# Optimization experiments

Measured on AMD Instinct MI355X. Metric: run time of the kernel, lower is better.

## Reference

```python
import jax, jax.numpy as jnp
import numpy as np

HEADS = 4
DIM_HEAD = 64
SCALE = 8.0
EPS = 1e-5  # fp32 branch of the original LayerNorm


def setup_inputs() -> dict:
    key = jax.random.key(0)
    k1, k2, k3 = jax.random.split(key, 3)
    B, C, F, H, W = 2, 256, 4, 32, 32
    inner = HEADS * DIM_HEAD  # 256
    x = jax.random.normal(k1, (B, C, F, H, W), dtype=jnp.float32)
    gamma = jnp.ones((1, C, 1, 1, 1), dtype=jnp.float32)
    w_qkv = jax.random.normal(k2, (3 * inner, C), dtype=jnp.float32) * 0.05
    w_out = jax.random.normal(k3, (C, inner), dtype=jnp.float32) * 0.05
    return {"x": x, "gamma": gamma, "w_qkv": w_qkv, "w_out": w_out}


def _l2norm(t):
    return t / jnp.sqrt(jnp.sum(t * t, axis=-1, keepdims=True) + 1e-12)


def reference(x, gamma, w_qkv, w_out):
    B, C, F, H, W = x.shape
    N = F * H * W
    inner = HEADS * DIM_HEAD
    residual = x

    # channel LayerNorm (biased variance over dim=1)
    mean = jnp.mean(x, axis=1, keepdims=True)
    var = jnp.mean((x - mean) ** 2, axis=1, keepdims=True)
    xn = (x - mean) / jnp.sqrt(var + EPS) * gamma

    # 1x1x1 conv == channel matmul; flatten spatial dims to sequence
    xn_flat = xn.reshape(B, C, N)                      # [B, C, N]
    qkv = jnp.einsum('oc,bcn->bon', w_qkv, xn_flat)    # [B, 3*inner, N]
    qkv = qkv.reshape(B, 3, HEADS, DIM_HEAD, N)        # chunk then split heads
    qkv = jnp.transpose(qkv, (1, 0, 2, 4, 3))          # [3, B, h, N, d]
    q, k, v = qkv[0], qkv[1], qkv[2]

    q = _l2norm(q)
    k = _l2norm(k)

    sim = jnp.einsum('bhid,bhjd->bhij', q, k) * SCALE  # [B, h, N, N]
    attn = jax.nn.softmax(sim, axis=-1)
    out = jnp.einsum('bhij,bhjd->bhid', attn, v)       # [B, h, N, d]

    # 'b h n d -> b (h d) n' then 1x1x1 out conv
    out = jnp.transpose(out, (0, 1, 3, 2)).reshape(B, inner, N)
    out = jnp.einsum('oi,bin->bon', w_out, out).reshape(B, C, F, H, W)
    return out + residual
```

## Files before the change

### kernel.cpp

```cpp
#include <hip/hip_runtime.h>

#define BATCH 2
#define CCH   256
#define NSEQ  4096
#define NH    4
#define DH    64
#define INNER 256

typedef __attribute__((ext_vector_type(8))) __bf16 bf16x8;
typedef __attribute__((ext_vector_type(4))) float f32x4;
typedef __attribute__((ext_vector_type(8))) unsigned short u16x8;
typedef __attribute__((ext_vector_type(4))) unsigned short u16x4;

#define GLD16(gsrc, ldst)                                                     \
  __builtin_amdgcn_global_load_lds(                                           \
      (const __attribute__((address_space(1))) unsigned int*)(const void*)(gsrc), \
      (__attribute__((address_space(3))) unsigned int*)(void*)(ldst), 16, 0, 0)

static __device__ __forceinline__ unsigned short f2bfr(float f) {
  union { float f; unsigned u; } v; v.f = f;
  return (unsigned short)((v.u + 0x8000u) >> 16);
}
static __device__ __forceinline__ unsigned pack2(float f0, float f1) {
  union { float f; unsigned u; } a, b; a.f = f0; b.f = f1;
  return __builtin_amdgcn_perm(b.u + 0x8000u, a.u + 0x8000u, 0x07060302u);
}
static __device__ __forceinline__ unsigned cvtpk(float lo, float hi) {
  unsigned r;
  asm("v_cvt_pk_bf16_f32 %0, %1, %2" : "=v"(r) : "v"(lo), "v"(hi));
  return r;
}
static __device__ __forceinline__ float bf2f(unsigned short u) {
  union { unsigned u; float f; } v; v.u = ((unsigned)u) << 16;
  return v.f;
}
static __device__ __forceinline__ bf16x8 ldb(const unsigned short* p) {
  return *(const bf16x8*)p;
}
static __device__ __forceinline__ f32x4 mm(bf16x8 a, bf16x8 b, f32x4 c) {
  return __builtin_amdgcn_mfma_f32_16x16x32_bf16(a, b, c, 0, 0, 0);
}
static __device__ __forceinline__ float ex2(float x) {
  return __builtin_amdgcn_exp2f(x);
}

__global__ __launch_bounds__(256) void k_lncvt(const float* __restrict__ x,
                                               const float* __restrict__ gamma,
                                               unsigned short* __restrict__ xn,
                                               const float* __restrict__ wq,
                                               const float* __restrict__ wo,
                                               unsigned short* __restrict__ wqb,
                                               unsigned short* __restrict__ wob) {
  int blk = blockIdx.x;
  if (blk >= 256) {
    int t = (blk - 256) * 256 + threadIdx.x;
    int e = t * 4;
    if (e < 768 * 256) {
      float4 v = *(const float4*)(wq + e);
      u16x4 pk = { f2bfr(v.x), f2bfr(v.y), f2bfr(v.z), f2bfr(v.w) };
      *(u16x4*)(wqb + e) = pk;
    } else {
      int e2 = e - 768 * 256;
      float4 v = *(const float4*)(wo + e2);
      u16x4 pk = { f2bfr(v.x), f2bfr(v.y), f2bfr(v.z), f2bfr(v.w) };
      *(u16x4*)(wob + e2) = pk;
    }
    return;
  }
  int b  = blk >> 7;
  int n0 = (blk & 127) * 32;
  int t  = threadIdx.x;
  int nl = t & 31;
  int cg = t >> 5;
  int n  = n0 + nl;
  const float* xp = x + ((size_t)(b * CCH + cg * 32)) * NSEQ + n;
  float vals[32];
  float s = 0.f, s2 = 0.f;
#pragma unroll
  for (int j = 0; j < 32; j++) {
    float v = xp[(size_t)j * NSEQ];
    vals[j] = v; s += v; s2 += v * v;
  }
  __shared__ float rs[8][32], rs2[8][32];
  rs[cg][nl] = s; rs2[cg][nl] = s2;
  __syncthreads();
  float S = 0.f, S2 = 0.f;
#pragma unroll
  for (int g = 0; g < 8; g++) { S += rs[g][nl]; S2 += rs2[g][nl]; }
  float mean = S * (1.f / 256.f);
  float var  = S2 * (1.f / 256.f) - mean * mean;
  float rstd = rsqrtf(var + 1e-5f);
  unsigned short* dst = xn + ((size_t)b * NSEQ + n) * CCH + cg * 32;
#pragma unroll
  for (int j0 = 0; j0 < 32; j0 += 8) {
    u16x8 pk;
#pragma unroll
    for (int j = 0; j < 8; j++)
      pk[j] = f2bfr((vals[j0 + j] - mean) * rstd * gamma[cg * 32 + j0 + j]);
    *(u16x8*)(dst + j0) = pk;
  }
}

__global__ __launch_bounds__(256) void k_qkv(const unsigned short* __restrict__ wqb,
                                             const unsigned short* __restrict__ xn,
                                             unsigned short* __restrict__ qkv,
                                             unsigned short* __restrict__ qt,
                                             unsigned short* __restrict__ ktb) {
  int n0 = blockIdx.x * 64;
  int oi = blockIdx.y;
  int o0 = oi * 64;
  int b  = blockIdx.z;
  __shared__ unsigned short Al[64 * 128];
  __shared__ unsigned short Bl[64 * 128];
  int t = threadIdx.x;
  int lane = t & 63, w = t >> 6;
  int c = lane & 15, quad = lane >> 4;
  int wm = w >> 1, wn = w & 1;
  f32x4 acc[2][2] = {};
  int lr = lane >> 4;
  int lchk = lane & 15;
  const unsigned short* apg = wqb + (size_t)o0 * CCH;
  const unsigned short* bpg = xn + ((size_t)b * NSEQ + n0) * CCH;
  for (int kt = 0; kt < 2; kt++) {
    if (kt) __syncthreads();
#pragma unroll
    for (int q = 0; q < 4; q++) {
      int r = w * 16 + q * 4 + lr;
      int srcoff = r * CCH + kt * 128 + ((lchk ^ (r & 7)) * 8);
      GLD16(apg + srcoff, Al + (size_t)(w * 16 + q * 4) * 128);
      GLD16(bpg + srcoff, Bl + (size_t)(w * 16 + q * 4) * 128);
    }
    __syncthreads();
#pragma unroll
    for (int ks = 0; ks < 4; ks++) {
      int ra0 = wm * 32 + c, ra1 = ra0 + 16;
      int rb0 = wn * 32 + c, rb1 = rb0 + 16;
      bf16x8 a0 = ldb(&Al[ra0 * 128 + (((ks * 4 + quad) ^ (ra0 & 7)) * 8)]);
      bf16x8 a1 = ldb(&Al[ra1 * 128 + (((ks * 4 + quad) ^ (ra1 & 7)) * 8)]);
      bf16x8 b0 = ldb(&Bl[rb0 * 128 + (((ks * 4 + quad) ^ (rb0 & 7)) * 8)]);
      bf16x8 b1 = ldb(&Bl[rb1 * 128 + (((ks * 4 + quad) ^ (rb1 & 7)) * 8)]);
      acc[0][0] = mm(a0, b0, acc[0][0]);
      acc[0][1] = mm(a0, b1, acc[0][1]);
      acc[1][0] = mm(a1, b0, acc[1][0]);
      acc[1][1] = mm(a1, b1, acc[1][1]);
    }
  }
  if (oi < 8) {
    float* sq = (float*)Al;
    float s0 = 0.f, s1 = 0.f;
#pragma unroll
    for (int i = 0; i < 2; i++)
#pragma unroll
      for (int rr = 0; rr < 4; rr++) {
        s0 += acc[i][0][rr] * acc[i][0][rr];
        s1 += acc[i][1][rr] * acc[i][1][rr];
      }
    s0 += __shfl_xor(s0, 16); s0 += __shfl_xor(s0, 32);
    s1 += __shfl_xor(s1, 16); s1 += __shfl_xor(s1, 32);
    __syncthreads();
    if (quad == 0) {
      sq[wm * 64 + wn * 32 + c]      = s0;
      sq[wm * 64 + wn * 32 + 16 + c] = s1;
    }
    __syncthreads();
    float r0 = rsqrtf(sq[wn * 32 + c]      + sq[64 + wn * 32 + c]      + 1e-12f);
    float r1 = rsqrtf(sq[wn * 32 + 16 + c] + sq[64 + wn * 32 + 16 + c] + 1e-12f);
    if (oi < 4) { r0 *= 11.541560327111707f; r1 *= 11.541560327111707f; }
    int h = oi & 3;
    unsigned short* base = (oi < 4 ? qt : ktb) + ((size_t)(b * NH + h) * NSEQ) * DH;
#pragma unroll
    for (int i = 0; i < 2; i++)
#pragma unroll
      for (int j = 0; j < 2; j++) {
        float rsc = j ? r1 : r0;
        int n = n0 + wn * 32 + j * 16 + c;
        int d = wm * 32 + i * 16 + quad * 4;
        uint2 pk = { pack2(acc[i][j][0] * rsc, acc[i][j][1] * rsc),
                     pack2(acc[i][j][2] * rsc, acc[i][j][3] * rsc) };
        *(uint2*)(base + (size_t)n * DH + d) = pk;
      }
  } else {
#pragma unroll
    for (int i = 0; i < 2; i++)
#pragma unroll
      for (int j = 0; j < 2; j++)
#pragma unroll
        for (int rr = 0; rr < 4; rr++) {
          int o = o0 + wm * 32 + i * 16 + quad * 4 + rr;
          int n = n0 + wn * 32 + j * 16 + c;
          qkv[((size_t)b * 768 + o) * NSEQ + n] = f2bfr(acc[i][j][rr]);
        }
  }
}

__global__ __launch_bounds__(256, 2) void k_attn(
    const unsigned short* __restrict__ qt,
    const unsigned short* __restrict__ ktb,
    const unsigned short* __restrict__ qkv,
    unsigned short* __restrict__ opart,
    float* __restrict__ lpart,
    int S, int kvlen) {
  int i0 = blockIdx.x * 256;
  int h  = blockIdx.y;
  int bz = blockIdx.z;
  int b  = bz / S, s = bz % S;
  __shared__ unsigned short Kl[2][64 * 64];
  __shared__ unsigned short Vl[2][64 * 64];
  int t = threadIdx.x;
  int lane = t & 63, w = t >> 6;
  int c = lane & 15, quad = lane >> 4;

  const unsigned short* qbase = qt  + ((size_t)(b * NH + h) * NSEQ) * DH;
  const unsigned short* kbase = ktb + ((size_t)(b * NH + h) * NSEQ) * DH;
  const unsigned short* vbase = qkv + ((size_t)b * 768 + 512 + h * 64) * NSEQ;

  bf16x8 qa[4], qb[4];
#pragma unroll
  for (int ss = 0; ss < 4; ss++) {
    const unsigned short* qp =
        qbase + (size_t)(i0 + w * 64 + ss * 16 + c) * DH + quad * 8;
    qa[ss] = ldb(qp); qb[ss] = ldb(qp + 32);
  }

  u16x8 onesu;
#pragma unroll
  for (int j = 0; j < 8; j++) onesu[j] = 0x3F80;
  bf16x8 ones = *(bf16x8*)&onesu;

  f32x4 acc[4][4] = {};
  f32x4 accl[4]  = {};

  int slr = lane >> 3, slc = lane & 7;
  int ssw_v  = (slc ^ slr) * 8;
  int ssw_k1 = (slc ^ (slr & 3)) * 8;
  int ssw_k2 = ssw_k1 ^ 32;
  const unsigned short* kp = kbase + (size_t)(s * kvlen + w * 16 + slr) * DH;
  const unsigned short* vp = vbase + (size_t)(w * 16 + slr) * NSEQ + s * kvlen + ssw_v;
  int sw0 = (quad ^ (c & 7)) * 8;
  int sw1 = sw0 ^ 32;
  int fK    = (c & 3) | (((c >> 2) & 1) << 2);
  int swk0  = (quad ^ fK) * 8;
  int swk1  = swk0 ^ 32;
  int krow0 = (c >> 2) * 8 + (c & 3);

  int nIt = kvlen / 64;
  GLD16(kp + ssw_k1,          &Kl[0][(w * 16)     * 64]);
  GLD16(kp + 8 * DH + ssw_k2, &Kl[0][(w * 16 + 8) * 64]);
  kp += 64 * DH;

  union U4 { unsigned u[4]; bf16x8 v; };
  U4 pA0[4], pA1[4], pB0[4], pB1[4];

#define QKSET(qA, qB, P0, P1)                                                 \
  {                                                                           \
    f32x4 z0 = {}, z1 = {}, z2 = {}, z3 = {};                                 \
    __builtin_amdgcn_s_setprio(1);                                            \
    z0 = mm(k00, qA, z0); z0 = mm(k01, qB, z0);                               \
    z1 = mm(k10, qA, z1); z1 = mm(k11, qB, z1);                               \
    z2 = mm(k20, qA, z2); z2 = mm(k21, qB, z2);                               \
    z3 = mm(k30, qA, z3); z3 = mm(k31, qB, z3);                               \
    __builtin_amdgcn_s_setprio(0);                                            \
    P0.u[0] = cvtpk(ex2(z0[0]), ex2(z0[1]));                                  \
    P0.u[1] = cvtpk(ex2(z0[2]), ex2(z0[3]));                                  \
    P0.u[2] = cvtpk(ex2(z1[0]), ex2(z1[1]));                                  \
    P0.u[3] = cvtpk(ex2(z1[2]), ex2(z1[3]));                                  \
    P1.u[0] = cvtpk(ex2(z2[0]), ex2(z2[1]));                                  \
    P1.u[1] = cvtpk(ex2(z2[2]), ex2(z2[3]));                                  \
    P1.u[2] = cvtpk(ex2(z3[0]), ex2(z3[1]));                                  \
    P1.u[3] = cvtpk(ex2(z3[2]), ex2(z3[3]));                                  \
  }

#define PVD(dt, Vb, PO0, PO1)                                                 \
  {                                                                           \
    bf16x8 v0 = ldb(&Vb[((dt) * 16 + c) * 64 + sw0]);                         \
    bf16x8 v1 = ldb(&Vb[((dt) * 16 + c) * 64 + sw1]);                         \
    __builtin_amdgcn_s_setprio(1);                                            \
    acc[0][dt] = mm(PO0[0].v, v0, acc[0][dt]);                                \
    acc[0][dt] = mm(PO1[0].v, v1, acc[0][dt]);                                \
    acc[1][dt] = mm(PO0[1].v, v0, acc[1][dt]);                                \
    acc[1][dt] = mm(PO1[1].v, v1, acc[1][dt]);                                \
    acc[2][dt] = mm(PO0[2].v, v0, acc[2][dt]);                                \
    acc[2][dt] = mm(PO1[2].v, v1, acc[2][dt]);                                \
    acc[3][dt] = mm(PO0[3].v, v0, acc[3][dt]);                                \
    acc[3][dt] = mm(PO1[3].v, v1, acc[3][dt]);                                \
    __builtin_amdgcn_s_setprio(0);                                            \
  }

#define ACCL(PO0, PO1)                                                        \
  __builtin_amdgcn_s_setprio(1);                                              \
  accl[0] = mm(PO0[0].v, ones, accl[0]); accl[0] = mm(PO1[0].v, ones, accl[0]); \
  accl[1] = mm(PO0[1].v, ones, accl[1]); accl[1] = mm(PO1[1].v, ones, accl[1]); \
  accl[2] = mm(PO0[2].v, ones, accl[2]); accl[2] = mm(PO1[2].v, ones, accl[2]); \
  accl[3] = mm(PO0[3].v, ones, accl[3]); accl[3] = mm(PO1[3].v, ones, accl[3]); \
  __builtin_amdgcn_s_setprio(0);

#define ITER(IT, PN0, PN1, PO0, PO1, DO_PV)                                   \
  {                                                                           \
    __syncthreads();    \
    if ((IT) + 1 < nIt) {                                                     \
      unsigned short* kd = &Kl[((IT) + 1) & 1][0];                            \
      GLD16(kp + ssw_k1,          kd + (w * 16) * 64);                        \
      GLD16(kp + 8 * DH + ssw_k2, kd + (w * 16 + 8) * 64);                    \
      kp += 64 * DH;                                                          \
    }                                                                         \
    {                                                                         \
      unsigned short* vd = &Vl[(IT) & 1][0];                                  \
      GLD16(vp,            vd + (w * 16) * 64);                               \
      GLD16(vp + 8 * NSEQ, vd + (w * 16 + 8) * 64);                           \
      vp += 64;                                                               \
    }                                                                         \
    const unsigned short* Kb = &Kl[(IT) & 1][0];                              \
    const unsigned short* Vb = &Vl[((IT) + 1) & 1][0];       \
    bf16x8 k00 = ldb(&Kb[(krow0)      * 64 + swk0]);                          \
    bf16x8 k01 = ldb(&Kb[(krow0)      * 64 + swk1]);                          \
    bf16x8 k10 = ldb(&Kb[(krow0 + 4)  * 64 + swk0]);                          \
    bf16x8 k11 = ldb(&Kb[(krow0 + 4)  * 64 + swk1]);                          \
    bf16x8 k20 = ldb(&Kb[(krow0 + 32) * 64 + swk0]);                          \
    bf16x8 k21 = ldb(&Kb[(krow0 + 32) * 64 + swk1]);                          \
    bf16x8 k30 = ldb(&Kb[(krow0 + 36) * 64 + swk0]);                          \
    bf16x8 k31 = ldb(&Kb[(krow0 + 36) * 64 + swk1]);                          \
    QKSET(qa[0], qb[0], PN0[0], PN1[0]);                                      \
    if (DO_PV) PVD(0, Vb, PO0, PO1);                                          \
    QKSET(qa[1], qb[1], PN0[1], PN1[1]);                                      \
    if (DO_PV) PVD(1, Vb, PO0, PO1);                                          \
    QKSET(qa[2], qb[2], PN0[2], PN1[2]);                                      \
    if (DO_PV) PVD(2, Vb, PO0, PO1);                                          \
    QKSET(qa[3], qb[3], PN0[3], PN1[3]);                                      \
    if (DO_PV) PVD(3, Vb, PO0, PO1);                                          \
    if (DO_PV) { ACCL(PO0, PO1); }                                            \
  }

  for (int itp = 0; itp < nIt / 2; ++itp) {
    int it0 = itp * 2;
    ITER(it0,     pA0, pA1, pB0, pB1, (itp > 0));
    ITER(it0 + 1, pB0, pB1, pA0, pA1, 1);
  }
  __syncthreads();
  {
    const unsigned short* Vb = &Vl[1][0];
    PVD(0, Vb, pB0, pB1);
    PVD(1, Vb, pB0, pB1);
    PVD(2, Vb, pB0, pB1);
    PVD(3, Vb, pB0, pB1);
    ACCL(pB0, pB1);
  }
#undef ITER
#undef ACCL
#undef PVD
#undef QKSET

  size_t rb = ((size_t)(b * NH + h) * S + s) * NSEQ + i0 + w * 64;
#pragma unroll
  for (int ss = 0; ss < 4; ss++) {
    size_t rbs = rb + ss * 16;
    if (c == 0) {
#pragma unroll
      for (int rr = 0; rr < 4; rr++)
        lpart[rbs + quad * 4 + rr] = accl[ss][rr];
    }
#pragma unroll
    for (int rr = 0; rr < 4; rr++)
#pragma unroll
      for (int dt = 0; dt < 4; dt++)
        opart[(rbs + quad * 4 + rr) * 64 + dt * 16 + c] = f2bfr(acc[ss][dt][rr]);
  }
}

__global__ __launch_bounds__(256) void k_out(const unsigned short* __restrict__ wob,
                                             const unsigned short* __restrict__ opart,
                                             const float* __restrict__ lpart,
                                             const float* __restrict__ x,
                                             float* __restrict__ out, int S) {
  int n0 = blockIdx.x * 64;
  int o0 = blockIdx.y * 64;
  int b  = blockIdx.z;
  __shared__ unsigned short Al[64 * 256];
  __shared__ unsigned short Bl[64 * 256];
  int t = threadIdx.x;
  int lane = t & 63, w = t >> 6;
  int c = lane & 15, quad = lane >> 4;
  int wm = w >> 1, wn = w & 1;
  int lr2 = lane >> 5, lch = lane & 31;
  const unsigned short* apg = wob + (size_t)o0 * INNER;
#pragma unroll
  for (int q = 0; q < 8; q++) {
    int r = w * 16 + q * 2 + lr2;
    int srcoff = r * INNER + ((lch ^ (r & 7)) * 8);
    GLD16(apg + srcoff, Al + (size_t)(w * 16 + q * 2) * 256);
  }
  int n_l = t >> 2;
  int seg = t & 3;
#pragma unroll
  for (int hh = 0; hh < 4; hh++) {
    float l = 0.f;
    float o[16];
#pragma unroll
    for (int j = 0; j < 16; j++) o[j] = 0.f;
    for (int s = 0; s < S; s++) {
      size_t rbm = ((size_t)(b * NH + hh) * S + s) * NSEQ + n0 + n_l;
      l += lpart[rbm];
      const unsigned short* p = opart + rbm * 64 + seg * 16;
      u16x8 v0 = *(const u16x8*)p;
      u16x8 v1 = *(const u16x8*)(p + 8);
#pragma unroll
      for (int j = 0; j < 8; j++) {
        o[j]     += bf2f(v0[j]);
        o[8 + j] += bf2f(v1[j]);
      }
    }
    float inv = 1.f / l;
    int cc = hh * 8 + seg * 2;
    uint4 pkA = { pack2(o[0] * inv,  o[1] * inv),  pack2(o[2] * inv,  o[3] * inv),
                  pack2(o[4] * inv,  o[5] * inv),  pack2(o[6] * inv,  o[7] * inv) };
    uint4 pkB = { pack2(o[8] * inv,  o[9] * inv),  pack2(o[10] * inv, o[11] * inv),
                  pack2(o[12] * inv, o[13] * inv), pack2(o[14] * inv, o[15] * inv) };
    *(uint4*)&Bl[n_l * 256 + (((cc)     ^ (n_l & 7)) * 8)] = pkA;
    *(uint4*)&Bl[n_l * 256 + (((cc + 1) ^ (n_l & 7)) * 8)] = pkB;
  }
  __syncthreads();
  f32x4 acc[2][2] = {};
#pragma unroll
  for (int ks = 0; ks < 8; ks++) {
    int ra0 = wm * 32 + c, ra1 = ra0 + 16;
    int rb0 = wn * 32 + c, rb1 = rb0 + 16;
    bf16x8 a0 = ldb(&Al[ra0 * 256 + (((ks * 4 + quad) ^ (ra0 & 7)) * 8)]);
    bf16x8 a1 = ldb(&Al[ra1 * 256 + (((ks * 4 + quad) ^ (ra1 & 7)) * 8)]);
    bf16x8 b0 = ldb(&Bl[rb0 * 256 + (((ks * 4 + quad) ^ (rb0 & 7)) * 8)]);
    bf16x8 b1 = ldb(&Bl[rb1 * 256 + (((ks * 4 + quad) ^ (rb1 & 7)) * 8)]);
    acc[0][0] = mm(a0, b0, acc[0][0]);
    acc[0][1] = mm(a0, b1, acc[0][1]);
    acc[1][0] = mm(a1, b0, acc[1][0]);
    acc[1][1] = mm(a1, b1, acc[1][1]);
  }
#pragma unroll
  for (int i = 0; i < 2; i++)
#pragma unroll
    for (int j = 0; j < 2; j++)
#pragma unroll
      for (int rr = 0; rr < 4; rr++) {
        int o = o0 + wm * 32 + i * 16 + quad * 4 + rr;
        int n = n0 + wn * 32 + j * 16 + c;
        size_t idx = ((size_t)b * CCH + o) * NSEQ + n;
        out[idx] = acc[i][j][rr] + x[idx];
      }
}

extern "C" void kernel_launch(void* const* d_in, const int* in_sizes, int n_in,
                              void* d_out, int out_size, void* d_ws, size_t ws_size,
                              hipStream_t stream) {
  const float* x     = (const float*)d_in[0];
  const float* gamma = (const float*)d_in[1];
  const float* wq    = (const float*)d_in[2];
  const float* wo    = (const float*)d_in[3];
  float* out = (float*)d_out;

  const size_t MB = 1u << 20;
  char* ws = (char*)d_ws;
  unsigned short* xn  = (unsigned short*)(ws + 4 * MB);
  unsigned short* qkv = (unsigned short*)(ws + 8 * MB);
  unsigned short* wqb = (unsigned short*)(ws + 20 * MB);
  unsigned short* wob = (unsigned short*)(ws + 20 * MB + 512 * 1024);
  unsigned short* qt  = (unsigned short*)(ws + 21 * MB);
  unsigned short* ktb = (unsigned short*)(ws + 25 * MB);
  unsigned short* opart = (unsigned short*)(ws + 29 * MB);
  int S;
  if (ws_size >= 48 * MB) S = 4;
  else if (ws_size >= 40 * MB) S = 2;
  else S = 1;
  size_t opart_bytes = (size_t)S * BATCH * NH * NSEQ * DH * 2;
  float* lpart = (float*)(ws + 29 * MB + opart_bytes);
  int kvlen = NSEQ / S;

  k_lncvt<<<dim3(512),          256, 0, stream>>>(x, gamma, xn, wq, wo, wqb, wob);
  k_qkv  <<<dim3(64, 12, 2),    256, 0, stream>>>(wqb, xn, qkv, qt, ktb);
  k_attn <<<dim3(16, 4, 2 * S), 256, 0, stream>>>(qt, ktb, qkv, opart,
                                                  lpart, S, kvlen);
  k_out  <<<dim3(64, 4, 2),     256, 0, stream>>>(wob, opart, lpart, x, out, S);
}
```

Measured before the change: 128.1 us.

## Split split-KV merge into separate kernel and drop setprio hints in attention

Moves the split-KV partial merge and normalization out of the output projection kernel into a new k_merge kernel. k_merge writes a bf16 [B, N, inner] attention output to workspace. Previously each of the 4 output-channel blocks redid the merge for its tile. k_out now streams both operands with global_load_lds in two K-chunks, using half the shared memory. The change also removes the s_setprio raise/lower around the MFMA groups in the attention kernel, and adds one launch plus an intermediate round trip through memory.

```diff
diff --git a/kernel.cpp b/kernel.cpp
--- a/kernel.cpp
+++ b/kernel.cpp
@@ -254,12 +254,10 @@
 #define QKSET(qA, qB, P0, P1)                                                 \
   {                                                                           \
     f32x4 z0 = {}, z1 = {}, z2 = {}, z3 = {};                                 \
-    __builtin_amdgcn_s_setprio(1);                                            \
     z0 = mm(k00, qA, z0); z0 = mm(k01, qB, z0);                               \
     z1 = mm(k10, qA, z1); z1 = mm(k11, qB, z1);                               \
     z2 = mm(k20, qA, z2); z2 = mm(k21, qB, z2);                               \
     z3 = mm(k30, qA, z3); z3 = mm(k31, qB, z3);                               \
-    __builtin_amdgcn_s_setprio(0);                                            \
     P0.u[0] = cvtpk(ex2(z0[0]), ex2(z0[1]));                                  \
     P0.u[1] = cvtpk(ex2(z0[2]), ex2(z0[3]));                                  \
     P0.u[2] = cvtpk(ex2(z1[0]), ex2(z1[1]));                                  \
@@ -274,7 +272,6 @@
   {                                                                           \
     bf16x8 v0 = ldb(&Vb[((dt) * 16 + c) * 64 + sw0]);                         \
     bf16x8 v1 = ldb(&Vb[((dt) * 16 + c) * 64 + sw1]);                         \
-    __builtin_amdgcn_s_setprio(1);                                            \
     acc[0][dt] = mm(PO0[0].v, v0, acc[0][dt]);                                \
     acc[0][dt] = mm(PO1[0].v, v1, acc[0][dt]);                                \
     acc[1][dt] = mm(PO0[1].v, v0, acc[1][dt]);                                \
@@ -283,16 +280,13 @@
     acc[2][dt] = mm(PO1[2].v, v1, acc[2][dt]);                                \
     acc[3][dt] = mm(PO0[3].v, v0, acc[3][dt]);                                \
     acc[3][dt] = mm(PO1[3].v, v1, acc[3][dt]);                                \
-    __builtin_amdgcn_s_setprio(0);                                            \
   }
 
 #define ACCL(PO0, PO1)                                                        \
-  __builtin_amdgcn_s_setprio(1);                                              \
   accl[0] = mm(PO0[0].v, ones, accl[0]); accl[0] = mm(PO1[0].v, ones, accl[0]); \
   accl[1] = mm(PO0[1].v, ones, accl[1]); accl[1] = mm(PO1[1].v, ones, accl[1]); \
   accl[2] = mm(PO0[2].v, ones, accl[2]); accl[2] = mm(PO1[2].v, ones, accl[2]); \
-  accl[3] = mm(PO0[3].v, ones, accl[3]); accl[3] = mm(PO1[3].v, ones, accl[3]); \
-  __builtin_amdgcn_s_setprio(0);
+  accl[3] = mm(PO0[3].v, ones, accl[3]); accl[3] = mm(PO1[3].v, ones, accl[3]);
 
 #define ITER(IT, PN0, PN1, PO0, PO1, DO_PV)                                   \
   {                                                                           \
@@ -366,71 +360,83 @@
   }
 }
 
+__global__ __launch_bounds__(256) void k_merge(
+    const unsigned short* __restrict__ opart,
+    const float* __restrict__ lpart,
+    unsigned short* __restrict__ ao, int S) {
+  int t = blockIdx.x * 256 + threadIdx.x;
+  int row = t >> 2;
+  int dseg = (t & 3) * 16;
+  int b = row >> 14, rem = row & 16383;
+  int h = rem >> 12, i = rem & 4095;
+
+  float l = 0.f;
+  float o[16];
+#pragma unroll
+  for (int j = 0; j < 16; j++) o[j] = 0.f;
+  for (int s = 0; s < S; s++) {
+    size_t rb = ((size_t)(b * NH + h) * S + s) * NSEQ + i;
+    l += lpart[rb];
+    const unsigned short* p = opart + rb * 64 + dseg;
+    u16x8 v0 = *(const u16x8*)p;
+    u16x8 v1 = *(const u16x8*)(p + 8);
+#pragma unroll
+    for (int j = 0; j < 8; j++) {
+      o[j]     += bf2f(v0[j]);
+      o[8 + j] += bf2f(v1[j]);
+    }
+  }
+  float inv = 1.f / l;
+  unsigned short* dst = ao + ((size_t)b * NSEQ + i) * INNER + h * 64 + dseg;
+  uint4 pk0 = { pack2(o[0] * inv, o[1] * inv),  pack2(o[2] * inv, o[3] * inv),
+                pack2(o[4] * inv, o[5] * inv),  pack2(o[6] * inv, o[7] * inv) };
+  uint4 pk1 = { pack2(o[8] * inv, o[9] * inv),  pack2(o[10] * inv, o[11] * inv),
+                pack2(o[12] * inv, o[13] * inv),pack2(o[14] * inv, o[15] * inv) };
+  *(uint4*)dst = pk0;
+  *(uint4*)(dst + 8) = pk1;
+}
+
 __global__ __launch_bounds__(256) void k_out(const unsigned short* __restrict__ wob,
-                                             const unsigned short* __restrict__ opart,
-                                             const float* __restrict__ lpart,
+                                             const unsigned short* __restrict__ ao,
                                              const float* __restrict__ x,
-                                             float* __restrict__ out, int S) {
+                                             float* __restrict__ out) {
   int n0 = blockIdx.x * 64;
   int o0 = blockIdx.y * 64;
   int b  = blockIdx.z;
-  __shared__ unsigned short Al[64 * 256];
-  __shared__ unsigned short Bl[64 * 256];
+  __shared__ unsigned short Al[64 * 128];
+  __shared__ unsigned short Bl[64 * 128];
   int t = threadIdx.x;
   int lane = t & 63, w = t >> 6;
   int c = lane & 15, quad = lane >> 4;
   int wm = w >> 1, wn = w & 1;
-  int lr2 = lane >> 5, lch = lane & 31;
+  f32x4 acc[2][2] = {};
+  int lr = lane >> 4;
+  int lchk = lane & 15;
   const unsigned short* apg = wob + (size_t)o0 * INNER;
-#pragma unroll
-  for (int q = 0; q < 8; q++) {
-    int r = w * 16 + q * 2 + lr2;
-    int srcoff = r * INNER + ((lch ^ (r & 7)) * 8);
-    GLD16(apg + srcoff, Al + (size_t)(w * 16 + q * 2) * 256);
-  }
-  int n_l = t >> 2;
-  int seg = t & 3;
-#pragma unroll
-  for (int hh = 0; hh < 4; hh++) {
-    float l = 0.f;
-    float o[16];
-#pragma unroll
-    for (int j = 0; j < 16; j++) o[j] = 0.f;
-    for (int s = 0; s < S; s++) {
-      size_t rbm = ((size_t)(b * NH + hh) * S + s) * NSEQ + n0 + n_l;
-      l += lpart[rbm];
-      const unsigned short* p = opart + rbm * 64 + seg * 16;
-      u16x8 v0 = *(const u16x8*)p;
-      u16x8 v1 = *(const u16x8*)(p + 8);
-#pragma unroll
-      for (int j = 0; j < 8; j++) {
-        o[j]     += bf2f(v0[j]);
-        o[8 + j] += bf2f(v1[j]);
-      }
-    }
-    float inv = 1.f / l;
-    int cc = hh * 8 + seg * 2;
-    uint4 pkA = { pack2(o[0] * inv,  o[1] * inv),  pack2(o[2] * inv,  o[3] * inv),
-                  pack2(o[4] * inv,  o[5] * inv),  pack2(o[6] * inv,  o[7] * inv) };
-    uint4 pkB = { pack2(o[8] * inv,  o[9] * inv),  pack2(o[10] * inv, o[11] * inv),
-                  pack2(o[12] * inv, o[13] * inv), pack2(o[14] * inv, o[15] * inv) };
-    *(uint4*)&Bl[n_l * 256 + (((cc)     ^ (n_l & 7)) * 8)] = pkA;
-    *(uint4*)&Bl[n_l * 256 + (((cc + 1) ^ (n_l & 7)) * 8)] = pkB;
-  }
-  __syncthreads();
-  f32x4 acc[2][2] = {};
-#pragma unroll
-  for (int ks = 0; ks < 8; ks++) {
-    int ra0 = wm * 32 + c, ra1 = ra0 + 16;
-    int rb0 = wn * 32 + c, rb1 = rb0 + 16;
-    bf16x8 a0 = ldb(&Al[ra0 * 256 + (((ks * 4 + quad) ^ (ra0 & 7)) * 8)]);
-    bf16x8 a1 = ldb(&Al[ra1 * 256 + (((ks * 4 + quad) ^ (ra1 & 7)) * 8)]);
-    bf16x8 b0 = ldb(&Bl[rb0 * 256 + (((ks * 4 + quad) ^ (rb0 & 7)) * 8)]);
-    bf16x8 b1 = ldb(&Bl[rb1 * 256 + (((ks * 4 + quad) ^ (rb1 & 7)) * 8)]);
-    acc[0][0] = mm(a0, b0, acc[0][0]);
-    acc[0][1] = mm(a0, b1, acc[0][1]);
-    acc[1][0] = mm(a1, b0, acc[1][0]);
-    acc[1][1] = mm(a1, b1, acc[1][1]);
+  const unsigned short* bpg = ao + ((size_t)b * NSEQ + n0) * INNER;
+  for (int kt = 0; kt < 2; kt++) {
+    if (kt) __syncthreads();
+#pragma unroll
+    for (int q = 0; q < 4; q++) {
+      int r = w * 16 + q * 4 + lr;
+      int srcoff = r * INNER + kt * 128 + ((lchk ^ (r & 7)) * 8);
+      GLD16(apg + srcoff, Al + (size_t)(w * 16 + q * 4) * 128);
+      GLD16(bpg + srcoff, Bl + (size_t)(w * 16 + q * 4) * 128);
+    }
+    __syncthreads();
+#pragma unroll
+    for (int ks = 0; ks < 4; ks++) {
+      int ra0 = wm * 32 + c, ra1 = ra0 + 16;
+      int rb0 = wn * 32 + c, rb1 = rb0 + 16;
+      bf16x8 a0 = ldb(&Al[ra0 * 128 + (((ks * 4 + quad) ^ (ra0 & 7)) * 8)]);
+      bf16x8 a1 = ldb(&Al[ra1 * 128 + (((ks * 4 + quad) ^ (ra1 & 7)) * 8)]);
+      bf16x8 b0 = ldb(&Bl[rb0 * 128 + (((ks * 4 + quad) ^ (rb0 & 7)) * 8)]);
+      bf16x8 b1 = ldb(&Bl[rb1 * 128 + (((ks * 4 + quad) ^ (rb1 & 7)) * 8)]);
+      acc[0][0] = mm(a0, b0, acc[0][0]);
+      acc[0][1] = mm(a0, b1, acc[0][1]);
+      acc[1][0] = mm(a1, b0, acc[1][0]);
+      acc[1][1] = mm(a1, b1, acc[1][1]);
+    }
   }
 #pragma unroll
   for (int i = 0; i < 2; i++)
@@ -456,6 +462,7 @@
 
   const size_t MB = 1u << 20;
   char* ws = (char*)d_ws;
+  unsigned short* ao  = (unsigned short*)ws;
   unsigned short* xn  = (unsigned short*)(ws + 4 * MB);
   unsigned short* qkv = (unsigned short*)(ws + 8 * MB);
   unsigned short* wqb = (unsigned short*)(ws + 20 * MB);
@@ -475,5 +482,6 @@
   k_qkv  <<<dim3(64, 12, 2),    256, 0, stream>>>(wqb, xn, qkv, qt, ktb);
   k_attn <<<dim3(16, 4, 2 * S), 256, 0, stream>>>(qt, ktb, qkv, opart,
                                                   lpart, S, kvlen);
-  k_out  <<<dim3(64, 4, 2),     256, 0, stream>>>(wob, opart, lpart, x, out, S);
-}
+  k_merge<<<dim3(512),          256, 0, stream>>>(opart, lpart, ao, S);
+  k_out  <<<dim3(64, 4, 2),     256, 0, stream>>>(wob, ao, x, out);
+}
```

Result: faster. 123.3 us (-3.7%).
